# Performance work log

Hardware: AMD Instinct MI355X
Metric: run time of the kernel (lower is better)

## Reference

```python
import jax, jax.numpy as jnp
import numpy as np
import math

B, H, S, DIM = 1, 16, 2048, 128

def _clin(xr, xi, wr, wi, br, bi):
    # complex linear: F.linear semantics -> x @ W.T
    out_r = xr @ wr.T - xi @ wi.T + br
    out_i = xr @ wi.T + xi @ wr.T + bi
    return out_r, out_i

def setup_inputs() -> dict:
    key = jax.random.key(0)
    ks = jax.random.split(key, 32)
    shp = (B, H, S, DIM)
    names = ["q_r", "q_i", "k_r", "k_i", "v_r", "v_i", "pe_q_r", "pe_q_i", "pe_k_r", "pe_k_i"]
    d = {n: jax.random.normal(ks[i], shp, jnp.float32) for i, n in enumerate(names)}
    wscale = 1.0 / math.sqrt(DIM)
    i = 10
    for p in ["q", "k", "v", "g", "o"]:
        d[p + "w_r"] = jax.random.normal(ks[i], (DIM, DIM), jnp.float32) * wscale; i += 1
        d[p + "w_i"] = jax.random.normal(ks[i], (DIM, DIM), jnp.float32) * wscale; i += 1
        d[p + "b_r"] = jnp.zeros((DIM,), jnp.float32)
        d[p + "b_i"] = jnp.zeros((DIM,), jnp.float32)
    return d

def reference(q_r, q_i, k_r, k_i, v_r, v_i, pe_q_r, pe_q_i, pe_k_r, pe_k_i,
              qw_r, qw_i, qb_r, qb_i, kw_r, kw_i, kb_r, kb_i,
              vw_r, vw_i, vb_r, vb_i, gw_r, gw_i, gb_r, gb_i,
              ow_r, ow_i, ob_r, ob_i):
    scale = DIM ** -0.5
    qr, qi = _clin(q_r, q_i, qw_r, qw_i, qb_r, qb_i)
    kr, ki = _clin(k_r, k_i, kw_r, kw_i, kb_r, kb_i)
    vr, vi = _clin(v_r, v_i, vw_r, vw_i, vb_r, vb_i)
    qr = qr + pe_q_r; qi = qi + pe_q_i
    kr = kr + pe_k_r; ki = ki + pe_k_i
    # complex QK^H -> real/imag parts, shapes [B,H,S,S]
    sr = jnp.einsum('bhqd,bhkd->bhqk', qr, kr) + jnp.einsum('bhqd,bhkd->bhqk', qi, ki)
    si = jnp.einsum('bhqd,bhkd->bhqk', qi, kr) - jnp.einsum('bhqd,bhkd->bhqk', qr, ki)
    scores = jnp.sqrt(sr * sr + si * si + 1e-8) * scale  # magnitude scores
    attn = jax.nn.softmax(scores, axis=-1)
    ar = attn @ vr
    ai = attn @ vi
    gr, gi = _clin(q_r, q_i, gw_r, gw_i, gb_r, gb_i)  # gate from raw q
    gar = gr * ar - gi * ai
    gai = gr * ai + gi * ar
    out_r, out_i = _clin(gar, gai, ow_r, ow_i, ob_r, ob_i)
    return (out_r, out_i, gr, gi)
```

## Files before the change

kernel.cpp:

```cpp
#include <hip/hip_runtime.h>
#include <math.h>

#define HH 16
#define SS 2048
#define DD 128
#define NROWS (HH * SS)
#define OUTSZ (HH * SS * DD)

typedef __attribute__((ext_vector_type(8))) short bf16x8;
typedef __attribute__((ext_vector_type(4))) float f32x4;
typedef __attribute__((ext_vector_type(8))) unsigned short u16x8;

#define MFMA16(a, b, c) __builtin_amdgcn_mfma_f32_16x16x32_bf16(a, b, c, 0, 0, 0)

__device__ __forceinline__ unsigned short f2bf(float f) {
    unsigned u = __float_as_uint(f);
    return (unsigned short)((u + 0x7FFFu + ((u >> 16) & 1u)) >> 16);
}
__device__ __forceinline__ bf16x8 negf(bf16x8 a) {
    bf16x8 r;
#pragma unroll
    for (int j = 0; j < 8; ++j) r[j] = (short)(a[j] ^ (short)0x8000);
    return r;
}

struct ClinPtrs {
    const float* xr; const float* xi;
    const float* gr; const float* gi;
    const float* wr; const float* wi;
    const float* br; const float* bi;
    const float* per; const float* pei;
    void* yr; void* yi;
    int outbf;
};

template <int TILES, bool GATE>
__global__ __launch_bounds__(512, 4)
void clin_half(ClinPtrs P0, ClinPtrs P1, ClinPtrs P2, ClinPtrs P3) {
    __shared__ unsigned short wsh[2][64][136];

    const int py = blockIdx.y;
    const ClinPtrs P = (py == 0) ? P0 : (py == 1) ? P1 : (py == 2) ? P2 : P3;

    const float* __restrict__ xr = P.xr;
    const float* __restrict__ xi = P.xi;
    const float* __restrict__ gr = P.gr;
    const float* __restrict__ gi = P.gi;
    const float* __restrict__ wr = P.wr;
    const float* __restrict__ wi = P.wi;
    const float* __restrict__ br = P.br;
    const float* __restrict__ bi = P.bi;
    const float* __restrict__ per = P.per;
    const float* __restrict__ pei = P.pei;

    const int t = threadIdx.x;
    const int w = t >> 6, lane = t & 63;
    const int lm = lane & 15, quad = lane >> 4;
    const int cb = blockIdx.z * 64;
    const long rowA = (long)blockIdx.x * (128 * TILES);
    const long tbase = rowA * DD + (long)(w * 16 + lm) * DD + quad * 8;

    float4 raw[2][4];
    {
        const long o = tbase;
        raw[0][0] = *(const float4*)(xr + o);
        raw[0][1] = *(const float4*)(xr + o + 4);
        raw[0][2] = *(const float4*)(xi + o);
        raw[0][3] = *(const float4*)(xi + o + 4);
    }

#pragma unroll
    for (int u = 0; u < 4; ++u) {
        const int f = t + 512 * u;
        const int c = f >> 10;
        const int rem = f & 1023;
        const int row = rem >> 4;
        const int g8 = (rem & 15) * 8;
        const float* src = (c ? wi : wr) + (long)(cb + row) * DD + g8;
        const float4 a = *(const float4*)src;
        const float4 b = *(const float4*)(src + 4);
        unsigned short tmp[8] = {f2bf(a.x), f2bf(a.y), f2bf(a.z), f2bf(a.w),
                                 f2bf(b.x), f2bf(b.y), f2bf(b.z), f2bf(b.w)};
        *(u16x8*)&wsh[c][row][g8] = *(u16x8*)tmp;
    }
    __syncthreads();

    const f32x4 z = {0.f, 0.f, 0.f, 0.f};

#pragma unroll
    for (int tt = 0; tt < TILES; ++tt) {
        f32x4 Or[4], Oi[4];
#pragma unroll
        for (int nt = 0; nt < 4; ++nt) { Or[nt] = z; Oi[nt] = z; }

#pragma unroll
        for (int dk = 0; dk < 4; ++dk) {
            const int step = tt * 4 + dk;
            const int p = step & 1;
            if (step + 1 < TILES * 4) {
                const int ns = step + 1;
                const long o = tbase + (long)(ns >> 2) * 128 * DD + (ns & 3) * 32;
                raw[p ^ 1][0] = *(const float4*)(xr + o);
                raw[p ^ 1][1] = *(const float4*)(xr + o + 4);
                raw[p ^ 1][2] = *(const float4*)(xi + o);
                raw[p ^ 1][3] = *(const float4*)(xi + o + 4);
            }
            bf16x8 xrf, xif;
            {
                const float4 a0 = raw[p][0], a1 = raw[p][1];
                const float4 b0 = raw[p][2], b1 = raw[p][3];
                float fr[8] = {a0.x, a0.y, a0.z, a0.w, a1.x, a1.y, a1.z, a1.w};
                float fi[8] = {b0.x, b0.y, b0.z, b0.w, b1.x, b1.y, b1.z, b1.w};
                if (GATE) {
                    const long o = tbase + (long)tt * 128 * DD + dk * 32;
                    const float4 c0v = *(const float4*)(gr + o);
                    const float4 c1v = *(const float4*)(gr + o + 4);
                    const float4 d0v = *(const float4*)(gi + o);
                    const float4 d1v = *(const float4*)(gi + o + 4);
                    const float ur[8] = {c0v.x, c0v.y, c0v.z, c0v.w,
                                         c1v.x, c1v.y, c1v.z, c1v.w};
                    const float ui[8] = {d0v.x, d0v.y, d0v.z, d0v.w,
                                         d1v.x, d1v.y, d1v.z, d1v.w};
#pragma unroll
                    for (int j = 0; j < 8; ++j) {
                        const float pr = fr[j] * ur[j] - fi[j] * ui[j];
                        const float pi = fr[j] * ui[j] + fi[j] * ur[j];
                        fr[j] = pr; fi[j] = pi;
                    }
                }
#pragma unroll
                for (int j = 0; j < 8; ++j) {
                    xrf[j] = (short)f2bf(fr[j]);
                    xif[j] = (short)f2bf(fi[j]);
                }
            }
            const bf16x8 nxi = negf(xif);
            const int off = dk * 32 + quad * 8;
#pragma unroll
            for (int nt = 0; nt < 4; ++nt) {
                const bf16x8 wrf = *(bf16x8*)&wsh[0][nt * 16 + lm][off];
                const bf16x8 wif = *(bf16x8*)&wsh[1][nt * 16 + lm][off];
                Or[nt] = MFMA16(xrf, wrf, Or[nt]);
                Or[nt] = MFMA16(nxi, wif, Or[nt]);
                Oi[nt] = MFMA16(xrf, wif, Oi[nt]);
                Oi[nt] = MFMA16(xif, wrf, Oi[nt]);
            }
        }

        const long m0 = rowA + tt * 128 + w * 16;
#pragma unroll
        for (int nt = 0; nt < 4; ++nt) {
            const int c = cb + nt * 16 + lm;
            const float bra = br[c], bia = bi[c];
#pragma unroll
            for (int reg = 0; reg < 4; ++reg) {
                const long R = m0 + quad * 4 + reg;
                float vr = Or[nt][reg] + bra;
                float vi = Oi[nt][reg] + bia;
                if (per != nullptr) {
                    vr += per[R * DD + c];
                    vi += pei[R * DD + c];
                }
                if (P.outbf) {
                    ((unsigned short*)P.yr)[R * DD + c] = f2bf(vr);
                    ((unsigned short*)P.yi)[R * DD + c] = f2bf(vi);
                } else {
                    ((float*)P.yr)[R * DD + c] = vr;
                    ((float*)P.yi)[R * DD + c] = vi;
                }
            }
        }
    }
}

__global__ __launch_bounds__(512, 2)
void attn_mfma(const unsigned short* __restrict__ qr, const unsigned short* __restrict__ qi,
               const unsigned short* __restrict__ kr, const unsigned short* __restrict__ ki,
               const unsigned short* __restrict__ vr, const unsigned short* __restrict__ vi,
               float* __restrict__ out_r, float* __restrict__ out_i) {
    __shared__ unsigned short ks[2][2][32][136];
    __shared__ unsigned short vt[2][2][DD][40];
    __shared__ unsigned short ps[128][40];

    const int t = threadIdx.x;
    const int w = t >> 6, lane = t & 63;
    const int lm = lane & 15, quad = lane >> 4;

    const int bid = blockIdx.x;
    const int xcd = bid & 7;
    const int rr = bid >> 3;
    const int qt = rr & 15;
    const int h  = xcd + 8 * (rr >> 4);
    const long hbase = (long)h * SS * DD;
    const int q0 = qt * 128;
    const float scale = 0.08838834764831845f;

    int kC[2], kR[2], kG[2];
    const unsigned short* kp[2];
#pragma unroll
    for (int u = 0; u < 2; ++u) {
        const int f = t + 512 * u;
        kC[u] = f >> 9;
        kR[u] = (f & 511) >> 4;
        kG[u] = (f & 15) * 8;
        kp[u] = (kC[u] ? ki : kr) + hbase + (long)kR[u] * DD + kG[u];
    }
    const int vC = t >> 8;
    const int vS2 = (t & 15) * 2;
    const int vD8 = ((t >> 4) & 15) * 8;
    const unsigned short* vp = (vC ? vi : vr) + hbase + (long)vS2 * DD + vD8;

    u16x8 kA0, kA1, vA0, vA1;
    kA0 = *(const u16x8*)(kp[0]);
    kA1 = *(const u16x8*)(kp[1]);
    vA0 = *(const u16x8*)(vp);
    vA1 = *(const u16x8*)(vp + DD);

    bf16x8 qrf[4], qif[4];
    {
        const long rb = hbase + (long)(q0 + w * 16 + lm) * DD;
#pragma unroll
        for (int dk = 0; dk < 4; ++dk) {
            qrf[dk] = *(const bf16x8*)(qr + rb + dk * 32 + quad * 8);
            qif[dk] = *(const bf16x8*)(qi + rb + dk * 32 + quad * 8);
        }
    }

    f32x4 Or[8], Oi[8];
    const f32x4 z = {0.f, 0.f, 0.f, 0.f};
#pragma unroll
    for (int nt = 0; nt < 8; ++nt) { Or[nt] = z; Oi[nt] = z; }
    float l_st[4] = {0.f, 0.f, 0.f, 0.f};

#pragma unroll
    for (int u = 0; u < 2; ++u)
        *(u16x8*)&ks[0][kC[u]][kR[u]][kG[u]] = (u ? kA1 : kA0);
#pragma unroll
    for (int j = 0; j < 8; ++j) {
        const unsigned val = (unsigned)(unsigned short)vA0[j] |
                             ((unsigned)(unsigned short)vA1[j] << 16);
        *(unsigned*)&vt[0][vC][vD8 + j][vS2] = val;
    }
    __syncthreads();

    for (int kt = 0; kt < SS / 32; ++kt) {
        const int b = kt & 1;
        if (kt + 1 < SS / 32) {
            const long koff = (long)(kt + 1) * 32 * DD;
            kA0 = *(const u16x8*)(kp[0] + koff);
            kA1 = *(const u16x8*)(kp[1] + koff);
            vA0 = *(const u16x8*)(vp + koff);
            vA1 = *(const u16x8*)(vp + koff + DD);
        }

        f32x4 sr0 = z, sr1 = z, si0 = z, si1 = z;
#pragma unroll
        for (int dk = 0; dk < 4; ++dk) {
            const int off = dk * 32 + quad * 8;
            const bf16x8 kr0 = *(bf16x8*)&ks[b][0][lm][off];
            const bf16x8 ki0 = *(bf16x8*)&ks[b][1][lm][off];
            const bf16x8 kr1 = *(bf16x8*)&ks[b][0][16 + lm][off];
            const bf16x8 ki1 = *(bf16x8*)&ks[b][1][16 + lm][off];
            const bf16x8 nq = negf(qrf[dk]);
            sr0 = MFMA16(qrf[dk], kr0, sr0);  sr0 = MFMA16(qif[dk], ki0, sr0);
            si0 = MFMA16(qif[dk], kr0, si0);  si0 = MFMA16(nq, ki0, si0);
            sr1 = MFMA16(qrf[dk], kr1, sr1);  sr1 = MFMA16(qif[dk], ki1, sr1);
            si1 = MFMA16(qif[dk], kr1, si1);  si1 = MFMA16(nq, ki1, si1);
        }

#pragma unroll
        for (int reg = 0; reg < 4; ++reg) {
            const float s0 = __builtin_amdgcn_sqrtf(
                fmaf(sr0[reg], sr0[reg], fmaf(si0[reg], si0[reg], 1e-8f))) * scale;
            const float s1 = __builtin_amdgcn_sqrtf(
                fmaf(sr1[reg], sr1[reg], fmaf(si1[reg], si1[reg], 1e-8f))) * scale;
            const float p0 = __expf(s0);
            const float p1 = __expf(s1);
            l_st[reg] += p0 + p1;
            ps[w * 16 + quad * 4 + reg][lm]      = f2bf(p0);
            ps[w * 16 + quad * 4 + reg][16 + lm] = f2bf(p1);
        }

        const bf16x8 pf = *(bf16x8*)&ps[w * 16 + lm][quad * 8];
#pragma unroll
        for (int nt = 0; nt < 8; ++nt) {
            const bf16x8 vrf = *(bf16x8*)&vt[b][0][nt * 16 + lm][quad * 8];
            const bf16x8 vif = *(bf16x8*)&vt[b][1][nt * 16 + lm][quad * 8];
            Or[nt] = MFMA16(pf, vrf, Or[nt]);
            Oi[nt] = MFMA16(pf, vif, Oi[nt]);
        }

        if (kt + 1 < SS / 32) {
            __syncthreads();
#pragma unroll
            for (int u = 0; u < 2; ++u)
                *(u16x8*)&ks[b ^ 1][kC[u]][kR[u]][kG[u]] = (u ? kA1 : kA0);
#pragma unroll
            for (int j = 0; j < 8; ++j) {
                const unsigned val = (unsigned)(unsigned short)vA0[j] |
                                     ((unsigned)(unsigned short)vA1[j] << 16);
                *(unsigned*)&vt[b ^ 1][vC][vD8 + j][vS2] = val;
            }
            __syncthreads();
        }
    }

    float linv[4];
#pragma unroll
    for (int reg = 0; reg < 4; ++reg) {
        float l = l_st[reg];
#pragma unroll
        for (int off = 1; off < 16; off <<= 1) l += __shfl_xor(l, off);
        linv[reg] = 1.f / l;
    }
    const long ob = hbase + (long)(q0 + w * 16) * DD;
#pragma unroll
    for (int nt = 0; nt < 8; ++nt) {
        const int c = nt * 16 + lm;
#pragma unroll
        for (int reg = 0; reg < 4; ++reg) {
            const long R = ob + (long)(quad * 4 + reg) * DD + c;
            out_r[R] = Or[nt][reg] * linv[reg];
            out_i[R] = Oi[nt][reg] * linv[reg];
        }
    }
}

extern "C" void kernel_launch(void* const* d_in, const int* in_sizes, int n_in,
                              void* d_out, int out_size, void* d_ws, size_t ws_size,
                              hipStream_t stream) {
    const float* q_r    = (const float*)d_in[0];
    const float* q_i    = (const float*)d_in[1];
    const float* k_r    = (const float*)d_in[2];
    const float* k_i    = (const float*)d_in[3];
    const float* v_r    = (const float*)d_in[4];
    const float* v_i    = (const float*)d_in[5];
    const float* pe_q_r = (const float*)d_in[6];
    const float* pe_q_i = (const float*)d_in[7];
    const float* pe_k_r = (const float*)d_in[8];
    const float* pe_k_i = (const float*)d_in[9];
    const float* qw_r = (const float*)d_in[10];
    const float* qw_i = (const float*)d_in[11];
    const float* qb_r = (const float*)d_in[12];
    const float* qb_i = (const float*)d_in[13];
    const float* kw_r = (const float*)d_in[14];
    const float* kw_i = (const float*)d_in[15];
    const float* kb_r = (const float*)d_in[16];
    const float* kb_i = (const float*)d_in[17];
    const float* vw_r = (const float*)d_in[18];
    const float* vw_i = (const float*)d_in[19];
    const float* vb_r = (const float*)d_in[20];
    const float* vb_i = (const float*)d_in[21];
    const float* gw_r = (const float*)d_in[22];
    const float* gw_i = (const float*)d_in[23];
    const float* gb_r = (const float*)d_in[24];
    const float* gb_i = (const float*)d_in[25];
    const float* ow_r = (const float*)d_in[26];
    const float* ow_i = (const float*)d_in[27];
    const float* ob_r = (const float*)d_in[28];
    const float* ob_i = (const float*)d_in[29];

    float* out_r = (float*)d_out;
    float* out_i = out_r + (long)OUTSZ;
    float* g_r   = out_r + 2L * OUTSZ;
    float* g_i   = out_r + 3L * OUTSZ;

    unsigned short* ws = (unsigned short*)d_ws;
    unsigned short* pqr = ws + 0L * OUTSZ;
    unsigned short* pqi = ws + 1L * OUTSZ;
    unsigned short* pkr = ws + 2L * OUTSZ;
    unsigned short* pki = ws + 3L * OUTSZ;
    unsigned short* pvr = ws + 4L * OUTSZ;
    unsigned short* pvi = ws + 5L * OUTSZ;
    float* aw_r = (float*)(ws + 6L * OUTSZ);
    float* aw_i = aw_r + (long)OUTSZ;

    const dim3 blk(512);

    ClinPtrs P0 = {q_r, q_i, nullptr, nullptr, qw_r, qw_i, qb_r, qb_i,
                   pe_q_r, pe_q_i, pqr, pqi, 1};
    ClinPtrs P1 = {k_r, k_i, nullptr, nullptr, kw_r, kw_i, kb_r, kb_i,
                   pe_k_r, pe_k_i, pkr, pki, 1};
    ClinPtrs P2 = {v_r, v_i, nullptr, nullptr, vw_r, vw_i, vb_r, vb_i,
                   nullptr, nullptr, pvr, pvi, 1};
    ClinPtrs P3 = {q_r, q_i, nullptr, nullptr, gw_r, gw_i, gb_r, gb_i,
                   nullptr, nullptr, g_r, g_i, 0};

    clin_half<4, false><<<dim3(64, 4, 2), blk, 0, stream>>>(P0, P1, P2, P3);

    attn_mfma<<<dim3((SS / 128) * HH), blk, 0, stream>>>(
        pqr, pqi, pkr, pki, pvr, pvi, aw_r, aw_i);

    ClinPtrs PF = {aw_r, aw_i, g_r, g_i, ow_r, ow_i, ob_r, ob_i,
                   nullptr, nullptr, out_r, out_i, 0};
    clin_half<1, true><<<dim3(256, 1, 2), blk, 0, stream>>>(PF, PF, PF, PF);
}
```

Before: 449.6 us.

## Pre-convert inputs to bf16 and fuse gating into attention epilogue

Adds a conversion kernel that casts q/k/v inputs to bf16 once, so the projection kernel reads half-width activations (q read twice for q and gate) and drops per-step conversion. The complex gate multiply moves into the attention epilogue, which writes bf16 gated outputs instead of fp32 attention outputs. The output projection then reads bf16 directly. This adds an extra launch and extra traffic for the conversion pass, and borrows output buffer space as scratch before later overwriting it.

```diff
diff --git a/kernel.cpp b/kernel.cpp
--- a/kernel.cpp
+++ b/kernel.cpp
@@ -24,9 +24,28 @@
     return r;
 }
 
-struct ClinPtrs {
-    const float* xr; const float* xi;
-    const float* gr; const float* gi;
+__global__ __launch_bounds__(256)
+void conv6(const float* __restrict__ s0, const float* __restrict__ s1,
+           const float* __restrict__ s2, const float* __restrict__ s3,
+           const float* __restrict__ s4, const float* __restrict__ s5,
+           unsigned short* __restrict__ d0, unsigned short* __restrict__ d1,
+           unsigned short* __restrict__ d2, unsigned short* __restrict__ d3,
+           unsigned short* __restrict__ d4, unsigned short* __restrict__ d5) {
+    const long o = ((long)blockIdx.x * 256 + threadIdx.x) * 8;
+    const float* ss[6] = {s0, s1, s2, s3, s4, s5};
+    unsigned short* dd[6] = {d0, d1, d2, d3, d4, d5};
+#pragma unroll
+    for (int u = 0; u < 6; ++u) {
+        const float4 a = *(const float4*)(ss[u] + o);
+        const float4 b = *(const float4*)(ss[u] + o + 4);
+        unsigned short tmp[8] = {f2bf(a.x), f2bf(a.y), f2bf(a.z), f2bf(a.w),
+                                 f2bf(b.x), f2bf(b.y), f2bf(b.z), f2bf(b.w)};
+        *(u16x8*)(dd[u] + o) = *(u16x8*)tmp;
+    }
+}
+
+struct ClinBF {
+    const unsigned short* xr; const unsigned short* xi;
     const float* wr; const float* wi;
     const float* br; const float* bi;
     const float* per; const float* pei;
@@ -34,18 +53,16 @@
     int outbf;
 };
 
-template <int TILES, bool GATE>
+template <int TILES>
 __global__ __launch_bounds__(512, 4)
-void clin_half(ClinPtrs P0, ClinPtrs P1, ClinPtrs P2, ClinPtrs P3) {
+void clin_bf(ClinBF P0, ClinBF P1, ClinBF P2, ClinBF P3) {
     __shared__ unsigned short wsh[2][64][136];
 
     const int py = blockIdx.y;
-    const ClinPtrs P = (py == 0) ? P0 : (py == 1) ? P1 : (py == 2) ? P2 : P3;
-
-    const float* __restrict__ xr = P.xr;
-    const float* __restrict__ xi = P.xi;
-    const float* __restrict__ gr = P.gr;
-    const float* __restrict__ gi = P.gi;
+    const ClinBF P = (py == 0) ? P0 : (py == 1) ? P1 : (py == 2) ? P2 : P3;
+
+    const unsigned short* __restrict__ xr = P.xr;
+    const unsigned short* __restrict__ xi = P.xi;
     const float* __restrict__ wr = P.wr;
     const float* __restrict__ wi = P.wi;
     const float* __restrict__ br = P.br;
@@ -58,15 +75,13 @@
     const int lm = lane & 15, quad = lane >> 4;
     const int cb = blockIdx.z * 64;
     const long rowA = (long)blockIdx.x * (128 * TILES);
-    const long tbase = rowA * DD + (long)(w * 16 + lm) * DD + quad * 8;
-
-    float4 raw[2][4];
-    {
-        const long o = tbase;
-        raw[0][0] = *(const float4*)(xr + o);
-        raw[0][1] = *(const float4*)(xr + o + 4);
-        raw[0][2] = *(const float4*)(xi + o);
-        raw[0][3] = *(const float4*)(xi + o + 4);
+    const long abase = (rowA + w * 16 + lm) * DD + quad * 8;
+
+    u16x8 fA[8], fB[8];
+#pragma unroll
+    for (int dk = 0; dk < 4; ++dk) {
+        fA[dk]     = *(const u16x8*)(xr + abase + dk * 32);
+        fA[4 + dk] = *(const u16x8*)(xi + abase + dk * 32);
     }
 
 #pragma unroll
@@ -89,51 +104,25 @@
 
 #pragma unroll
     for (int tt = 0; tt < TILES; ++tt) {
+        u16x8* cur = (tt & 1) ? fB : fA;
+        u16x8* nxt = (tt & 1) ? fA : fB;
+        if (tt + 1 < TILES) {
+            const long o = abase + (long)(tt + 1) * 128 * DD;
+#pragma unroll
+            for (int dk = 0; dk < 4; ++dk) {
+                nxt[dk]     = *(const u16x8*)(xr + o + dk * 32);
+                nxt[4 + dk] = *(const u16x8*)(xi + o + dk * 32);
+            }
+        }
+
         f32x4 Or[4], Oi[4];
 #pragma unroll
         for (int nt = 0; nt < 4; ++nt) { Or[nt] = z; Oi[nt] = z; }
 
 #pragma unroll
         for (int dk = 0; dk < 4; ++dk) {
-            const int step = tt * 4 + dk;
-            const int p = step & 1;
-            if (step + 1 < TILES * 4) {
-                const int ns = step + 1;
-                const long o = tbase + (long)(ns >> 2) * 128 * DD + (ns & 3) * 32;
-                raw[p ^ 1][0] = *(const float4*)(xr + o);
-                raw[p ^ 1][1] = *(const float4*)(xr + o + 4);
-                raw[p ^ 1][2] = *(const float4*)(xi + o);
-                raw[p ^ 1][3] = *(const float4*)(xi + o + 4);
-            }
-            bf16x8 xrf, xif;
-            {
-                const float4 a0 = raw[p][0], a1 = raw[p][1];
-                const float4 b0 = raw[p][2], b1 = raw[p][3];
-                float fr[8] = {a0.x, a0.y, a0.z, a0.w, a1.x, a1.y, a1.z, a1.w};
-                float fi[8] = {b0.x, b0.y, b0.z, b0.w, b1.x, b1.y, b1.z, b1.w};
-                if (GATE) {
-                    const long o = tbase + (long)tt * 128 * DD + dk * 32;
-                    const float4 c0v = *(const float4*)(gr + o);
-                    const float4 c1v = *(const float4*)(gr + o + 4);
-                    const float4 d0v = *(const float4*)(gi + o);
-                    const float4 d1v = *(const float4*)(gi + o + 4);
-                    const float ur[8] = {c0v.x, c0v.y, c0v.z, c0v.w,
-                                         c1v.x, c1v.y, c1v.z, c1v.w};
-                    const float ui[8] = {d0v.x, d0v.y, d0v.z, d0v.w,
-                                         d1v.x, d1v.y, d1v.z, d1v.w};
-#pragma unroll
-                    for (int j = 0; j < 8; ++j) {
-                        const float pr = fr[j] * ur[j] - fi[j] * ui[j];
-                        const float pi = fr[j] * ui[j] + fi[j] * ur[j];
-                        fr[j] = pr; fi[j] = pi;
-                    }
-                }
-#pragma unroll
-                for (int j = 0; j < 8; ++j) {
-                    xrf[j] = (short)f2bf(fr[j]);
-                    xif[j] = (short)f2bf(fi[j]);
-                }
-            }
+            const bf16x8 xrf = *(bf16x8*)&cur[dk];
+            const bf16x8 xif = *(bf16x8*)&cur[4 + dk];
             const bf16x8 nxi = negf(xif);
             const int off = dk * 32 + quad * 8;
 #pragma unroll
@@ -177,7 +166,8 @@
 void attn_mfma(const unsigned short* __restrict__ qr, const unsigned short* __restrict__ qi,
                const unsigned short* __restrict__ kr, const unsigned short* __restrict__ ki,
                const unsigned short* __restrict__ vr, const unsigned short* __restrict__ vi,
-               float* __restrict__ out_r, float* __restrict__ out_i) {
+               const float* __restrict__ g_r, const float* __restrict__ g_i,
+               unsigned short* __restrict__ gar, unsigned short* __restrict__ gai) {
     __shared__ unsigned short ks[2][2][32][136];
     __shared__ unsigned short vt[2][2][DD][40];
     __shared__ unsigned short ps[128][40];
@@ -320,8 +310,12 @@
 #pragma unroll
         for (int reg = 0; reg < 4; ++reg) {
             const long R = ob + (long)(quad * 4 + reg) * DD + c;
-            out_r[R] = Or[nt][reg] * linv[reg];
-            out_i[R] = Oi[nt][reg] * linv[reg];
+            const float ar = Or[nt][reg] * linv[reg];
+            const float ai = Oi[nt][reg] * linv[reg];
+            const float g1 = g_r[R];
+            const float g2 = g_i[R];
+            gar[R] = f2bf(g1 * ar - g2 * ai);
+            gai[R] = f2bf(g1 * ai + g2 * ar);
         }
     }
 }
@@ -364,6 +358,7 @@
     float* out_i = out_r + (long)OUTSZ;
     float* g_r   = out_r + 2L * OUTSZ;
     float* g_i   = out_r + 3L * OUTSZ;
+    unsigned short* d0u = (unsigned short*)d_out;
 
     unsigned short* ws = (unsigned short*)d_ws;
     unsigned short* pqr = ws + 0L * OUTSZ;
@@ -372,26 +367,28 @@
     unsigned short* pki = ws + 3L * OUTSZ;
     unsigned short* pvr = ws + 4L * OUTSZ;
     unsigned short* pvi = ws + 5L * OUTSZ;
-    float* aw_r = (float*)(ws + 6L * OUTSZ);
-    float* aw_i = aw_r + (long)OUTSZ;
-
-    const dim3 blk(512);
-
-    ClinPtrs P0 = {q_r, q_i, nullptr, nullptr, qw_r, qw_i, qb_r, qb_i,
-                   pe_q_r, pe_q_i, pqr, pqi, 1};
-    ClinPtrs P1 = {k_r, k_i, nullptr, nullptr, kw_r, kw_i, kb_r, kb_i,
-                   pe_k_r, pe_k_i, pkr, pki, 1};
-    ClinPtrs P2 = {v_r, v_i, nullptr, nullptr, vw_r, vw_i, vb_r, vb_i,
-                   nullptr, nullptr, pvr, pvi, 1};
-    ClinPtrs P3 = {q_r, q_i, nullptr, nullptr, gw_r, gw_i, gb_r, gb_i,
-                   nullptr, nullptr, g_r, g_i, 0};
-
-    clin_half<4, false><<<dim3(64, 4, 2), blk, 0, stream>>>(P0, P1, P2, P3);
-
-    attn_mfma<<<dim3((SS / 128) * HH), blk, 0, stream>>>(
-        pqr, pqi, pkr, pki, pvr, pvi, aw_r, aw_i);
-
-    ClinPtrs PF = {aw_r, aw_i, g_r, g_i, ow_r, ow_i, ob_r, ob_i,
-                   nullptr, nullptr, out_r, out_i, 0};
-    clin_half<1, true><<<dim3(256, 1, 2), blk, 0, stream>>>(PF, PF, PF, PF);
-}
+    unsigned short* cvr = ws + 6L * OUTSZ;
+    unsigned short* cvi = ws + 7L * OUTSZ;
+    unsigned short* gar = ws + 8L * OUTSZ;
+    unsigned short* gai = ws + 9L * OUTSZ;
+    unsigned short* cqr = d0u + 0L * OUTSZ;
+    unsigned short* cqi = d0u + 1L * OUTSZ;
+    unsigned short* ckr = d0u + 2L * OUTSZ;
+    unsigned short* cki = d0u + 3L * OUTSZ;
+
+    conv6<<<dim3(OUTSZ / 8 / 256), dim3(256), 0, stream>>>(
+        q_r, q_i, k_r, k_i, v_r, v_i, cqr, cqi, ckr, cki, cvr, cvi);
+
+    ClinBF P0 = {cqr, cqi, qw_r, qw_i, qb_r, qb_i, pe_q_r, pe_q_i, pqr, pqi, 1};
+    ClinBF P1 = {ckr, cki, kw_r, kw_i, kb_r, kb_i, pe_k_r, pe_k_i, pkr, pki, 1};
+    ClinBF P2 = {cvr, cvi, vw_r, vw_i, vb_r, vb_i, nullptr, nullptr, pvr, pvi, 1};
+    ClinBF P3 = {cqr, cqi, gw_r, gw_i, gb_r, gb_i, nullptr, nullptr, g_r, g_i, 0};
+    clin_bf<4><<<dim3(64, 4, 2), dim3(512), 0, stream>>>(P0, P1, P2, P3);
+
+    attn_mfma<<<dim3((SS / 128) * HH), dim3(512), 0, stream>>>(
+        pqr, pqi, pkr, pki, pvr, pvi, g_r, g_i, gar, gai);
+
+    ClinBF PF = {gar, gai, ow_r, ow_i, ob_r, ob_i, nullptr, nullptr,
+                 out_r, out_i, 0};
+    clin_bf<1><<<dim3(256, 1, 2), dim3(512), 0, stream>>>(PF, PF, PF, PF);
+}
```

New measurement: 524.8 us. +16.7%, slower.
